# Kernel tuning notes

Measured on AMD Instinct MI355X. Metric: run time of the kernel, lower is better.

Reference implementation:

```python
import jax, jax.numpy as jnp
import numpy as np

W1 = W2 = W3 = 7  # window size


def _rel_pos_indices(w1, w2, w3):
    # Static relative-position index table, matching the torch buffer.
    g = np.stack(np.meshgrid(np.arange(w1), np.arange(w2), np.arange(w3), indexing='ij'))
    g = g.reshape(3, -1).T                      # (N, 3), N = w1*w2*w3
    rel = g[:, None, :] - g[None, :, :]         # (N, N, 3)
    rel[..., 0] += w1 - 1
    rel[..., 1] += w2 - 1
    rel[..., 2] += w3 - 1
    strides = np.array([(2 * w2 - 1) * (2 * w3 - 1), 2 * w3 - 1, 1])
    return jnp.asarray((rel * strides).sum(-1), dtype=jnp.int32)  # (N, N)


def setup_inputs() -> dict:
    key = jax.random.key(0)
    k1, k2, k3, k4 = jax.random.split(key, 4)
    dim, heads = 256, 8
    x = jax.random.normal(k1, (2, 4, 4, 4, W1, W2, W3, dim), dtype=jnp.float32)
    w_qkv = jax.random.normal(k2, (dim, 3 * dim), dtype=jnp.float32) * (dim ** -0.5)
    w_out = jax.random.normal(k3, (dim, dim), dtype=jnp.float32) * (dim ** -0.5)
    n_rel = (2 * W1 - 1) * (2 * W2 - 1) * (2 * W3 - 1)  # 2197
    rel_bias_table = jax.random.normal(k4, (n_rel, heads), dtype=jnp.float32) * 0.02
    return {"x": x, "w_qkv": w_qkv, "w_out": w_out, "rel_bias_table": rel_bias_table}


def reference(x, w_qkv, w_out, rel_bias_table):
    b, gx, gy, gz, w1, w2, w3, d = x.shape
    heads = rel_bias_table.shape[1]
    dh = d // heads
    scale = dh ** -0.5
    n = w1 * w2 * w3
    B = b * gx * gy * gz

    xf = x.reshape(B, n, d)
    qkv = xf @ w_qkv                             # (B, n, 3d)
    q, k, v = jnp.split(qkv, 3, axis=-1)

    def to_heads(t):
        return t.reshape(B, n, heads, dh).transpose(0, 2, 1, 3)  # (B, h, n, dh)

    q, k, v = to_heads(q), to_heads(k), to_heads(v)

    rel_idx = _rel_pos_indices(w1, w2, w3)                       # (n, n)
    bias = rel_bias_table[rel_idx].transpose(2, 0, 1)            # (h, n, n)

    logits = jnp.einsum('bhnd,bhmd->bhnm', q, k) * scale + bias[None]
    attn = jax.nn.softmax(logits, axis=-1)
    ctx = jnp.einsum('bhnm,bhmd->bhnd', attn, v)                 # (B, h, n, dh)

    out = ctx.transpose(0, 2, 1, 3).reshape(B, n, d) @ w_out     # (B, n, d)
    return out.reshape(b, gx, gy, gz, w1, w2, w3, d)
```

## Files before the change

kernel.cpp:

```cpp
#include <hip/hip_runtime.h>
#include <math.h>

using f16   = _Float16;
using f16x2 = __attribute__((ext_vector_type(2))) _Float16;
using f16x4 = __attribute__((ext_vector_type(4))) _Float16;
using f16x8 = __attribute__((ext_vector_type(8))) _Float16;
using f32x4 = __attribute__((ext_vector_type(4))) float;

#define NW    343
#define NWP   352
#define VTP   356
#define HEADS 8
#define MTOT  43904
#define LOG2E 1.4426950408889634f
#define QSC   (0.17677669529663687f * 1.4426950408889634f)

typedef const __attribute__((address_space(1))) unsigned int* gp1_t;
typedef __attribute__((address_space(3))) unsigned int* lp3_t;
__device__ __forceinline__ void gload_lds16(const void* g, void* l) {
    __builtin_amdgcn_global_load_lds((gp1_t)g, (lp3_t)l, 16, 0, 0);
}

__device__ __forceinline__ f16x2 pk_cvt(float a, float b) {
    return __builtin_bit_cast(f16x2, __builtin_amdgcn_cvt_pkrtz(a, b));
}

__device__ __forceinline__ float dot2acc(f16x2 a, float acc) {
#if __has_builtin(__builtin_amdgcn_fdot2)
    const f16x2 one2 = { (f16)1.f, (f16)1.f };
    return __builtin_amdgcn_fdot2(a, one2, acc, false);
#else
    return acc + (float)a[0] + (float)a[1];
#endif
}

__global__ void cvt_x(const float* __restrict__ x, f16* __restrict__ xb) {
    int id = blockIdx.x * 256 + threadIdx.x;
    float4 v = *(const float4*)(x + id * 4);
    f16x4 o = { (f16)v.x, (f16)v.y, (f16)v.z, (f16)v.w };
    *(f16x4*)(xb + id * 4) = o;
}

__global__ void cvt_wT(const float* __restrict__ W, f16* __restrict__ WT,
                       int N, int scaleN, float sc) {
    int id = blockIdx.x * 256 + threadIdx.x;
    int n = id >> 8, k = id & 255;
    float v = W[k * N + n];
    if (n < scaleN) v *= sc;
    WT[n * 256 + k] = (f16)v;
}

__global__ void bias_k(const float* __restrict__ tab, f16* __restrict__ bp) {
    int id = blockIdx.x * 256 + threadIdx.x;
    int h = id / (NWP * NWP);
    int rem = id - h * NWP * NWP;
    int i = rem / NWP, j = rem - (rem / NWP) * NWP;
    float v;
    if (j >= NW) v = 0.f;
    else if (i >= NW) v = 1.f;
    else {
        int a1 = i / 49, a2 = (i / 7) % 7, a3 = i % 7;
        int b1 = j / 49, b2 = (j / 7) % 7, b3 = j % 7;
        int idx = (a1 - b1 + 6) * 169 + (a2 - b2 + 6) * 13 + (a3 - b3 + 6);
        v = exp2f(tab[idx * 8 + h] * LOG2E);
    }
    bp[id] = (f16)v;
}

template<bool OUT_F32>
__launch_bounds__(256)
__global__ void gemm_k(const f16* __restrict__ A, const f16* __restrict__ Bt,
                       void* __restrict__ Cp, int N, int NT) {
    __shared__ f16 As[128 * 32];
    __shared__ f16 Bs[128 * 32];
    const int nwg = gridDim.x;
    const int bid = blockIdx.x;
    const int q8 = nwg >> 3, r8 = nwg & 7;
    const int xcd = bid & 7, pos = bid >> 3;
    const int wg = (xcd < r8 ? xcd * (q8 + 1) : r8 * (q8 + 1) + (xcd - r8) * q8) + pos;
    const int mt = wg / NT, nt = wg - mt * NT;
    const int m0 = mt * 128;
    const int n0 = nt * 128;
    const int t = threadIdx.x;
    const int wave = t >> 6, lane = t & 63;
    const int q = lane >> 4, c = lane & 15;
    const int wm = (wave >> 1) * 64, wn = (wave & 1) * 64;
    const int r0 = t >> 2;
    const int c8 = (t & 3) * 8;

    f32x4 acc[4][4] = {};
#pragma unroll
    for (int ks = 0; ks < 256; ks += 32) {
        gload_lds16(&A[(size_t)(m0 + r0) * 256 + ks + c8],        &As[r0 * 32 + c8]);
        gload_lds16(&A[(size_t)(m0 + r0 + 64) * 256 + ks + c8],   &As[(r0 + 64) * 32 + c8]);
        gload_lds16(&Bt[(size_t)(n0 + r0) * 256 + ks + c8],       &Bs[r0 * 32 + c8]);
        gload_lds16(&Bt[(size_t)(n0 + r0 + 64) * 256 + ks + c8],  &Bs[(r0 + 64) * 32 + c8]);
        __syncthreads();
        f16x8 af[4], bf[4];
#pragma unroll
        for (int a = 0; a < 4; a++) af[a] = *(const f16x8*)&As[(wm + a * 16 + c) * 32 + q * 8];
#pragma unroll
        for (int b = 0; b < 4; b++) bf[b] = *(const f16x8*)&Bs[(wn + b * 16 + c) * 32 + q * 8];
#pragma unroll
        for (int a = 0; a < 4; a++)
#pragma unroll
            for (int b = 0; b < 4; b++)
                acc[a][b] = __builtin_amdgcn_mfma_f32_16x16x32_f16(af[a], bf[b], acc[a][b], 0, 0, 0);
        __syncthreads();
    }
#pragma unroll
    for (int a = 0; a < 4; a++)
#pragma unroll
        for (int b = 0; b < 4; b++) {
            int row0 = m0 + wm + a * 16 + q * 4;
            int col = n0 + wn + b * 16 + c;
#pragma unroll
            for (int r = 0; r < 4; r++) {
                float v = acc[a][b][r];
                if (OUT_F32) ((float*)Cp)[(size_t)(row0 + r) * N + col] = v;
                else         ((f16*)Cp)[(size_t)(row0 + r) * N + col] = (f16)v;
            }
        }
}

template<bool HASB>
__device__ __forceinline__ void attn_tiles(
    const f16* __restrict__ qkv, const f16* __restrict__ ebH,
    f16* __restrict__ ctx, const f16* Ks, const f16* Vt,
    size_t base, int w, int h, int q, int c, int ta, int tb)
{
    const int iqa = ta * 16 + c;
    const int iqb = tb * 16 + c;
    const int iqac = iqa < NW ? iqa : NW - 1;
    const int iqbc = iqb < NW ? iqb : NW - 1;
    f16x8 qfa = *(const f16x8*)&qkv[base + (size_t)iqac * 768 + h * 32 + q * 8];
    f16x8 qfb{};
    if constexpr (HASB) qfb = *(const f16x8*)&qkv[base + (size_t)iqbc * 768 + h * 32 + q * 8];
    const f16* browA = ebH + (size_t)iqa * NWP;
    const f16* browB = ebH + (size_t)iqb * NWP;

    f32x4 o0a = {0.f,0.f,0.f,0.f}, o1a = {0.f,0.f,0.f,0.f};
    f32x4 o0b = {0.f,0.f,0.f,0.f}, o1b = {0.f,0.f,0.f,0.f};
    float lsa = 0.f, lsb = 0.f;
    const f32x4 z = {0.f, 0.f, 0.f, 0.f};
#pragma unroll
    for (int jt = 0; jt < NWP / 16; jt++) {
        const int jb = jt * 16;
        f16x8 kf = *(const f16x8*)&Ks[(jb + c) * 32 + q * 8];
        f16x4 v0 = *(const f16x4*)&Vt[c * VTP + jb + q * 4];
        f16x4 v1 = *(const f16x4*)&Vt[(16 + c) * VTP + jb + q * 4];

        f16x4 eba = *(const f16x4*)&browA[jb + q * 4];
        f32x4 sa = __builtin_amdgcn_mfma_f32_16x16x32_f16(kf, qfa, z, 0, 0, 0);
        f16x2 pla = pk_cvt(__builtin_amdgcn_exp2f(sa[0]), __builtin_amdgcn_exp2f(sa[1]));
        f16x2 pha = pk_cvt(__builtin_amdgcn_exp2f(sa[2]), __builtin_amdgcn_exp2f(sa[3]));
        f16x2 ela = { eba[0], eba[1] }, eha = { eba[2], eba[3] };
        pla *= ela; pha *= eha;
        lsa = dot2acc(pla, lsa);
        lsa = dot2acc(pha, lsa);
        f16x4 pfa = { pla[0], pla[1], pha[0], pha[1] };
        o0a = __builtin_amdgcn_mfma_f32_16x16x16f16(v0, pfa, o0a, 0, 0, 0);
        o1a = __builtin_amdgcn_mfma_f32_16x16x16f16(v1, pfa, o1a, 0, 0, 0);

        if constexpr (HASB) {
            f16x4 ebb = *(const f16x4*)&browB[jb + q * 4];
            f32x4 sb = __builtin_amdgcn_mfma_f32_16x16x32_f16(kf, qfb, z, 0, 0, 0);
            f16x2 plb = pk_cvt(__builtin_amdgcn_exp2f(sb[0]), __builtin_amdgcn_exp2f(sb[1]));
            f16x2 phb = pk_cvt(__builtin_amdgcn_exp2f(sb[2]), __builtin_amdgcn_exp2f(sb[3]));
            f16x2 elb = { ebb[0], ebb[1] }, ehb = { ebb[2], ebb[3] };
            plb *= elb; phb *= ehb;
            lsb = dot2acc(plb, lsb);
            lsb = dot2acc(phb, lsb);
            f16x4 pfb = { plb[0], plb[1], phb[0], phb[1] };
            o0b = __builtin_amdgcn_mfma_f32_16x16x16f16(v0, pfb, o0b, 0, 0, 0);
            o1b = __builtin_amdgcn_mfma_f32_16x16x16f16(v1, pfb, o1b, 0, 0, 0);
        }
    }
    lsa += __shfl_xor(lsa, 16);
    lsa += __shfl_xor(lsa, 32);
    if (iqa < NW) {
        float inv = 1.f / lsa;
        size_t ob = (size_t)(w * NW + iqa) * 256 + h * 32;
        f16x4 s0 = { (f16)(o0a[0] * inv), (f16)(o0a[1] * inv),
                     (f16)(o0a[2] * inv), (f16)(o0a[3] * inv) };
        f16x4 s1 = { (f16)(o1a[0] * inv), (f16)(o1a[1] * inv),
                     (f16)(o1a[2] * inv), (f16)(o1a[3] * inv) };
        *(f16x4*)&ctx[ob + q * 4] = s0;
        *(f16x4*)&ctx[ob + 16 + q * 4] = s1;
    }
    if constexpr (HASB) {
        lsb += __shfl_xor(lsb, 16);
        lsb += __shfl_xor(lsb, 32);
        if (iqb < NW) {
            float inv = 1.f / lsb;
            size_t ob = (size_t)(w * NW + iqb) * 256 + h * 32;
            f16x4 s0 = { (f16)(o0b[0] * inv), (f16)(o0b[1] * inv),
                         (f16)(o0b[2] * inv), (f16)(o0b[3] * inv) };
            f16x4 s1 = { (f16)(o1b[0] * inv), (f16)(o1b[1] * inv),
                         (f16)(o1b[2] * inv), (f16)(o1b[3] * inv) };
            *(f16x4*)&ctx[ob + q * 4] = s0;
            *(f16x4*)&ctx[ob + 16 + q * 4] = s1;
        }
    }
}

__launch_bounds__(256, 3)
__global__ void attn_k(const f16* __restrict__ qkv, const f16* __restrict__ ebP,
                       f16* __restrict__ ctx) {
    const int w = blockIdx.x >> 3;
    const int h = blockIdx.x & 7;
    __shared__ f16 Ks[NWP * 32];
    __shared__ f16 Vt[32 * VTP];
    const int t = threadIdx.x;
    const size_t base = (size_t)(w * NW) * 768;

    for (int u = t; u < NWP * 4; u += 256) {
        int row = u >> 2, un = u & 3;
        int rc = row < NW ? row : NW - 1;
        gload_lds16(&qkv[base + (size_t)rc * 768 + 256 + h * 32 + un * 8], &Ks[u * 8]);
    }
    for (int u = t; u < NWP * 4; u += 256) {
        int row = u >> 2, un = u & 3;
        if (row < NW) {
            uint4 val = *(const uint4*)&qkv[base + (size_t)row * 768 + 512 + h * 32 + un * 8];
            const f16* pv = (const f16*)&val;
#pragma unroll
            for (int e = 0; e < 8; e++) Vt[(un * 8 + e) * VTP + row] = pv[e];
        } else {
#pragma unroll
            for (int e = 0; e < 8; e++) Vt[(un * 8 + e) * VTP + row] = (f16)0.f;
        }
    }
    __syncthreads();

    const int wave = t >> 6, lane = t & 63;
    const int q = lane >> 4, c = lane & 15;
    const f16* ebH = ebP + (size_t)h * NWP * NWP;

#pragma unroll
    for (int pass = 0; pass < 3; pass++) {
        int p = wave + 4 * pass;
        if (p < 10)
            attn_tiles<true >(qkv, ebH, ctx, Ks, Vt, base, w, h, q, c, 2 * p, 2 * p + 1);
        else
            attn_tiles<false>(qkv, ebH, ctx, Ks, Vt, base, w, h, q, c, p + 10, p + 10);
    }
}

extern "C" void kernel_launch(void* const* d_in, const int* in_sizes, int n_in,
                              void* d_out, int out_size, void* d_ws, size_t ws_size,
                              hipStream_t stream) {
    const float* x    = (const float*)d_in[0];
    const float* wqkv = (const float*)d_in[1];
    const float* wout = (const float*)d_in[2];
    const float* tab  = (const float*)d_in[3];

    char* ws = (char*)d_ws;
    size_t off = 0;
    f16*   xb     = (f16*)(ws + off);   off += (size_t)MTOT * 256 * 2;
    f16*   wqkvT  = (f16*)(ws + off);   off += (size_t)768 * 256 * 2;
    f16*   woutT  = (f16*)(ws + off);   off += (size_t)256 * 256 * 2;
    f16*   ebP    = (f16*)(ws + off);   off += (size_t)8 * NWP * NWP * 2;
    f16*   qkvb   = (f16*)(ws + off);   off += (size_t)MTOT * 768 * 2;
    f16*   ctxb   = (f16*)(ws + off);   off += (size_t)MTOT * 256 * 2;
    if (ws_size < off) return;

    cvt_x <<<MTOT * 256 / 1024, 256, 0, stream>>>(x, xb);
    cvt_wT<<<768, 256, 0, stream>>>(wqkv, wqkvT, 768, 256, QSC);
    cvt_wT<<<256, 256, 0, stream>>>(wout, woutT, 256, 0, 1.f);
    bias_k<<<8 * NWP * NWP / 256, 256, 0, stream>>>(tab, ebP);
    gemm_k<false><<<MTOT / 128 * 6, 256, 0, stream>>>(xb, wqkvT, qkvb, 768, 6);
    attn_k<<<128 * HEADS, 256, 0, stream>>>(qkvb, ebP, ctxb);
    gemm_k<true><<<MTOT / 128 * 2, 256, 0, stream>>>(ctxb, woutT, d_out, 256, 2);
}
```

Before: 194.1 us.

## Fuse x fp16 conversion into QKV GEMM and merge prep kernels

Removes the standalone x-to-fp16 conversion kernel: the QKV GEMM now reads fp32 x directly, converts in registers and stores to LDS. The three small weight and bias prep kernels are merged into one launch. This saves a full write and read of the fp16 copy of x plus launch overhead. The trade-off is that the A tile in the QKV GEMM is reread as fp32 by every N-tile (6x), and the loads become synchronous register loads instead of async global-to-LDS loads.

```diff
diff --git a/kernel.cpp b/kernel.cpp
--- a/kernel.cpp
+++ b/kernel.cpp
@@ -34,42 +34,42 @@
 #endif
 }
 
-__global__ void cvt_x(const float* __restrict__ x, f16* __restrict__ xb) {
-    int id = blockIdx.x * 256 + threadIdx.x;
-    float4 v = *(const float4*)(x + id * 4);
-    f16x4 o = { (f16)v.x, (f16)v.y, (f16)v.z, (f16)v.w };
-    *(f16x4*)(xb + id * 4) = o;
-}
-
-__global__ void cvt_wT(const float* __restrict__ W, f16* __restrict__ WT,
-                       int N, int scaleN, float sc) {
-    int id = blockIdx.x * 256 + threadIdx.x;
-    int n = id >> 8, k = id & 255;
-    float v = W[k * N + n];
-    if (n < scaleN) v *= sc;
-    WT[n * 256 + k] = (f16)v;
-}
-
-__global__ void bias_k(const float* __restrict__ tab, f16* __restrict__ bp) {
-    int id = blockIdx.x * 256 + threadIdx.x;
-    int h = id / (NWP * NWP);
-    int rem = id - h * NWP * NWP;
-    int i = rem / NWP, j = rem - (rem / NWP) * NWP;
-    float v;
-    if (j >= NW) v = 0.f;
-    else if (i >= NW) v = 1.f;
-    else {
-        int a1 = i / 49, a2 = (i / 7) % 7, a3 = i % 7;
-        int b1 = j / 49, b2 = (j / 7) % 7, b3 = j % 7;
-        int idx = (a1 - b1 + 6) * 169 + (a2 - b2 + 6) * 13 + (a3 - b3 + 6);
-        v = exp2f(tab[idx * 8 + h] * LOG2E);
-    }
-    bp[id] = (f16)v;
-}
-
-template<bool OUT_F32>
+__global__ void prep_k(const float* __restrict__ wqkv, const float* __restrict__ wout,
+                       const float* __restrict__ tab,
+                       f16* __restrict__ wqkvT, f16* __restrict__ woutT,
+                       f16* __restrict__ ebP) {
+    int b = blockIdx.x;
+    if (b < 768) {
+        int id = b * 256 + threadIdx.x;
+        int n = id >> 8, k = id & 255;
+        float v = wqkv[k * 768 + n];
+        if (n < 256) v *= QSC;
+        wqkvT[n * 256 + k] = (f16)v;
+    } else if (b < 1024) {
+        int id = (b - 768) * 256 + threadIdx.x;
+        int n = id >> 8, k = id & 255;
+        woutT[n * 256 + k] = (f16)wout[k * 256 + n];
+    } else {
+        int id = (b - 1024) * 256 + threadIdx.x;
+        int h = id / (NWP * NWP);
+        int rem = id - h * NWP * NWP;
+        int i = rem / NWP, j = rem - (rem / NWP) * NWP;
+        float v;
+        if (j >= NW) v = 0.f;
+        else if (i >= NW) v = 1.f;
+        else {
+            int a1 = i / 49, a2 = (i / 7) % 7, a3 = i % 7;
+            int b1 = j / 49, b2 = (j / 7) % 7, b3 = j % 7;
+            int idx = (a1 - b1 + 6) * 169 + (a2 - b2 + 6) * 13 + (a3 - b3 + 6);
+            v = exp2f(tab[idx * 8 + h] * LOG2E);
+        }
+        ebP[id] = (f16)v;
+    }
+}
+
+template<bool OUT_F32, bool AF32>
 __launch_bounds__(256)
-__global__ void gemm_k(const f16* __restrict__ A, const f16* __restrict__ Bt,
+__global__ void gemm_k(const void* __restrict__ Ap, const f16* __restrict__ Bt,
                        void* __restrict__ Cp, int N, int NT) {
     __shared__ f16 As[128 * 32];
     __shared__ f16 Bs[128 * 32];
@@ -91,8 +91,23 @@
     f32x4 acc[4][4] = {};
 #pragma unroll
     for (int ks = 0; ks < 256; ks += 32) {
-        gload_lds16(&A[(size_t)(m0 + r0) * 256 + ks + c8],        &As[r0 * 32 + c8]);
-        gload_lds16(&A[(size_t)(m0 + r0 + 64) * 256 + ks + c8],   &As[(r0 + 64) * 32 + c8]);
+        if constexpr (AF32) {
+            const float* Af = (const float*)Ap;
+            float4 u0 = *(const float4*)&Af[(size_t)(m0 + r0) * 256 + ks + c8];
+            float4 u1 = *(const float4*)&Af[(size_t)(m0 + r0) * 256 + ks + c8 + 4];
+            float4 u2 = *(const float4*)&Af[(size_t)(m0 + r0 + 64) * 256 + ks + c8];
+            float4 u3 = *(const float4*)&Af[(size_t)(m0 + r0 + 64) * 256 + ks + c8 + 4];
+            f16x8 h0 = { (f16)u0.x, (f16)u0.y, (f16)u0.z, (f16)u0.w,
+                         (f16)u1.x, (f16)u1.y, (f16)u1.z, (f16)u1.w };
+            f16x8 h1 = { (f16)u2.x, (f16)u2.y, (f16)u2.z, (f16)u2.w,
+                         (f16)u3.x, (f16)u3.y, (f16)u3.z, (f16)u3.w };
+            *(f16x8*)&As[r0 * 32 + c8] = h0;
+            *(f16x8*)&As[(r0 + 64) * 32 + c8] = h1;
+        } else {
+            const f16* Af = (const f16*)Ap;
+            gload_lds16(&Af[(size_t)(m0 + r0) * 256 + ks + c8],      &As[r0 * 32 + c8]);
+            gload_lds16(&Af[(size_t)(m0 + r0 + 64) * 256 + ks + c8], &As[(r0 + 64) * 32 + c8]);
+        }
         gload_lds16(&Bt[(size_t)(n0 + r0) * 256 + ks + c8],       &Bs[r0 * 32 + c8]);
         gload_lds16(&Bt[(size_t)(n0 + r0 + 64) * 256 + ks + c8],  &Bs[(r0 + 64) * 32 + c8]);
         __syncthreads();
@@ -257,7 +272,6 @@
 
     char* ws = (char*)d_ws;
     size_t off = 0;
-    f16*   xb     = (f16*)(ws + off);   off += (size_t)MTOT * 256 * 2;
     f16*   wqkvT  = (f16*)(ws + off);   off += (size_t)768 * 256 * 2;
     f16*   woutT  = (f16*)(ws + off);   off += (size_t)256 * 256 * 2;
     f16*   ebP    = (f16*)(ws + off);   off += (size_t)8 * NWP * NWP * 2;
@@ -265,11 +279,9 @@
     f16*   ctxb   = (f16*)(ws + off);   off += (size_t)MTOT * 256 * 2;
     if (ws_size < off) return;
 
-    cvt_x <<<MTOT * 256 / 1024, 256, 0, stream>>>(x, xb);
-    cvt_wT<<<768, 256, 0, stream>>>(wqkv, wqkvT, 768, 256, QSC);
-    cvt_wT<<<256, 256, 0, stream>>>(wout, woutT, 256, 0, 1.f);
-    bias_k<<<8 * NWP * NWP / 256, 256, 0, stream>>>(tab, ebP);
-    gemm_k<false><<<MTOT / 128 * 6, 256, 0, stream>>>(xb, wqkvT, qkvb, 768, 6);
+    prep_k<<<1024 + 8 * NWP * NWP / 256, 256, 0, stream>>>(wqkv, wout, tab,
+                                                           wqkvT, woutT, ebP);
+    gemm_k<false, true ><<<MTOT / 128 * 6, 256, 0, stream>>>(x, wqkvT, qkvb, 768, 6);
     attn_k<<<128 * HEADS, 256, 0, stream>>>(qkvb, ebP, ctxb);
-    gemm_k<true><<<MTOT / 128 * 2, 256, 0, stream>>>(ctxb, woutT, d_out, 256, 2);
-}
+    gemm_k<true,  false><<<MTOT / 128 * 2, 256, 0, stream>>>(ctxb, woutT, d_out, 256, 2);
+}
```

Result: slower. 202.8 us (+4.5%).
